# Optimization experiments

Measured on AMD Instinct MI355X. Metric: run time of the kernel, lower is better.

The kernel has to match this reference:

```python
import jax, jax.numpy as jnp
import numpy as np

GAIN_CAP = 0.99
EPS = 1e-4


def _clamp(v):
    # clamp_preserve_grad(v, 0.0, cap) == cap - relu(cap - relu(v))
    r = jax.nn.relu
    return GAIN_CAP - r(GAIN_CAP - r(v))


def _pos(p):
    return jax.nn.softplus(p) + EPS


def setup_inputs() -> dict:
    key = jax.random.key(0)
    ks = jax.random.split(key, 12)
    B, C, H, W, O, M = 4, 128, 256, 256, 16, 32
    return {
        "x": jax.random.normal(ks[0], (B, C, H, W), jnp.float32),
        "steer": jax.random.normal(ks[1], (B, O, H, W), jnp.float32),
        "modulation": jax.random.normal(ks[2], (B, M), jnp.float32),
        "r_center": 0.1 * jax.random.normal(ks[3], (C,), jnp.float32),
        "r_horizontal": 0.1 * jax.random.normal(ks[4], (C,), jnp.float32),
        "r_vertical": 0.1 * jax.random.normal(ks[5], (C,), jnp.float32),
        "r_diag": 0.1 * jax.random.normal(ks[6], (C,), jnp.float32),
        "gain_horizontal": 0.1 * jax.random.normal(ks[7], (C,), jnp.float32),
        "gain_vertical": 0.1 * jax.random.normal(ks[8], (C,), jnp.float32),
        "gain_diag": 0.1 * jax.random.normal(ks[9], (C,), jnp.float32),
        "steer_w": 0.1 * jax.random.normal(ks[10], (4, O), jnp.float32),  # 1x1 conv weight squeezed
        "mod_w": 0.1 * jax.random.normal(ks[11], (3, M), jnp.float32),    # Linear(M,3,bias=False)
    }


def reference(x, steer, modulation, r_center, r_horizontal, r_vertical, r_diag,
              gain_horizontal, gain_vertical, gain_diag, steer_w, mod_w):
    cview = lambda p: p[None, :, None, None]  # (1,C,1,1)
    center = x
    right = jnp.roll(x, -1, axis=-1)
    left = jnp.roll(x, 1, axis=-1)
    up = jnp.roll(x, 1, axis=-2)
    down = jnp.roll(x, -1, axis=-2)
    diag_ne = jnp.roll(x, (-1, -1), axis=(-2, -1))
    diag_sw = jnp.roll(x, (1, 1), axis=(-2, -1))
    diag_nw = jnp.roll(x, (1, -1), axis=(-2, -1))
    diag_se = jnp.roll(x, (-1, 1), axis=(-2, -1))

    r_c = cview(_pos(r_center))
    r_h = cview(_pos(r_horizontal))
    r_v = cview(_pos(r_vertical))
    r_d = cview(_pos(r_diag))

    flow_h = (right - center + (left - center)) / (r_c + r_h)
    flow_v = (up - center + (down - center)) / (r_c + r_v)
    flow_d = (diag_ne - center + (diag_sw - center) + (diag_nw - center) + (diag_se - center)) / (2.0 * (r_c + r_d))

    gh = jnp.tanh(cview(gain_horizontal))
    gv = jnp.tanh(cview(gain_vertical))
    gd = jnp.tanh(cview(gain_diag))

    # modulation gating: [B,3] -> [B,3,1,1]
    delta = jnp.tanh(modulation @ mod_w.T)[:, :, None, None]
    gh = _clamp(gh * (1.0 + 0.1 * delta[:, 0:1]))
    gv = _clamp(gv * (1.0 + 0.1 * delta[:, 1:2]))
    gd = _clamp(gd * (1.0 + 0.1 * delta[:, 2:3]))

    # steer gating: 1x1 conv (no bias) then tanh -> [B,4,H,W]
    steer_fields = jnp.tanh(jnp.einsum('bohw,po->bphw', steer, steer_w))
    gh = _clamp(gh * (1.0 + 0.2 * steer_fields[:, 0:1]))
    gv = _clamp(gv * (1.0 + 0.2 * steer_fields[:, 1:2]))
    gd = _clamp(gd * (1.0 + 0.2 * steer_fields[:, 2:3]))

    update = gh * flow_h + gv * flow_v + gd * flow_d
    return center + update
```

## Files before the change

kernel.cpp:

```cpp
#include <hip/hip_runtime.h>
#include <math.h>

#define GAIN_CAP 0.99f
#define EPSV 1e-4f

static constexpr int B = 4, C = 128, H = 256, W = 256, O = 16, M = 32;
static constexpr int HW = H * W;

typedef float   vfloat4 __attribute__((ext_vector_type(4)));
typedef _Float16 half4v __attribute__((ext_vector_type(4)));
typedef _Float16 half8v __attribute__((ext_vector_type(8)));

static constexpr int SFP_FLOATS = B * HW * 2;
static constexpr int G_SZ = B * C * 3;

__device__ __forceinline__ float softplusf(float x) {
    return log1pf(expf(-fabsf(x))) + fmaxf(x, 0.0f);
}
__device__ __forceinline__ float clampg(float v) {
    return fminf(fmaxf(v, 0.0f), GAIN_CAP);
}
__device__ __forceinline__ float fast_tanh(float x) {
    float e = __expf(2.0f * x);
    return 1.0f - 2.0f * __builtin_amdgcn_rcpf(e + 1.0f);
}

__global__ void __launch_bounds__(256)
steer_kernel(const float* __restrict__ steer,
             const float* __restrict__ steer_w,
             const float* __restrict__ r_center,
             const float* __restrict__ r_h,
             const float* __restrict__ r_v,
             const float* __restrict__ r_d,
             const float* __restrict__ g_h,
             const float* __restrict__ g_v,
             const float* __restrict__ g_d,
             const float* __restrict__ modulation,
             const float* __restrict__ mod_w,
             half4v* __restrict__ sfp,
             float* __restrict__ gains,
             float* __restrict__ invd)
{
    if (blockIdx.x == 0 && threadIdx.x < C) {
        int c = threadIdx.x;
        float rc = softplusf(r_center[c]) + EPSV;
        invd[c * 3 + 0] = 1.0f / (rc + softplusf(r_h[c]) + EPSV);
        invd[c * 3 + 1] = 1.0f / (rc + softplusf(r_v[c]) + EPSV);
        invd[c * 3 + 2] = 1.0f / (2.0f * (rc + softplusf(r_d[c]) + EPSV));
        float th = tanhf(g_h[c]), tv = tanhf(g_v[c]), td = tanhf(g_d[c]);
        for (int b = 0; b < B; ++b) {
            float a0 = 0.f, a1 = 0.f, a2 = 0.f;
#pragma unroll
            for (int m = 0; m < M; ++m) {
                float mv = modulation[b * M + m];
                a0 += mv * mod_w[0 * M + m];
                a1 += mv * mod_w[1 * M + m];
                a2 += mv * mod_w[2 * M + m];
            }
            gains[(b * C + c) * 3 + 0] = clampg(th * (1.0f + 0.1f * tanhf(a0)));
            gains[(b * C + c) * 3 + 1] = clampg(tv * (1.0f + 0.1f * tanhf(a1)));
            gains[(b * C + c) * 3 + 2] = clampg(td * (1.0f + 0.1f * tanhf(a2)));
        }
    }

    int idx = blockIdx.x * 256 + threadIdx.x;
    int b   = idx >> 14;
    int g   = idx & 16383;
    const float4* sp = (const float4*)(steer + ((size_t)b * O << 16)) + g;

    float4 a0 = {0.f, 0.f, 0.f, 0.f}, a1 = a0, a2 = a0;
#pragma unroll
    for (int o = 0; o < O; ++o) {
        float4 v = sp[(size_t)o << 14];
        float w0 = steer_w[o], w1 = steer_w[O + o], w2 = steer_w[2 * O + o];
        a0.x += v.x * w0; a0.y += v.y * w0; a0.z += v.z * w0; a0.w += v.w * w0;
        a1.x += v.x * w1; a1.y += v.y * w1; a1.z += v.z * w1; a1.w += v.w * w1;
        a2.x += v.x * w2; a2.y += v.y * w2; a2.z += v.z * w2; a2.w += v.w * w2;
    }
    half8v oA, oB;
    oA[0] = (_Float16)fast_tanh(a0.x); oA[1] = (_Float16)fast_tanh(a1.x);
    oA[2] = (_Float16)fast_tanh(a2.x); oA[3] = (_Float16)0.f;
    oA[4] = (_Float16)fast_tanh(a0.y); oA[5] = (_Float16)fast_tanh(a1.y);
    oA[6] = (_Float16)fast_tanh(a2.y); oA[7] = (_Float16)0.f;
    oB[0] = (_Float16)fast_tanh(a0.z); oB[1] = (_Float16)fast_tanh(a1.z);
    oB[2] = (_Float16)fast_tanh(a2.z); oB[3] = (_Float16)0.f;
    oB[4] = (_Float16)fast_tanh(a0.w); oB[5] = (_Float16)fast_tanh(a1.w);
    oB[6] = (_Float16)fast_tanh(a2.w); oB[7] = (_Float16)0.f;
    half8v* op = (half8v*)sfp + ((size_t)idx << 1);
    op[0] = oA;
    op[1] = oB;
}

__device__ __forceinline__ vfloat4 row_compute(
    const float4& u, const float4& cc, const float4& d,
    float uL, float uR, float cL, float cR, float dL, float dR,
    float ih, float iv, float idg, float g0, float g1, float g2,
    const float (&s0)[4], const float (&s1)[4], const float (&s2)[4])
{
    float cA[4]  = {cc.x, cc.y, cc.z, cc.w};
    float uA[4]  = {u.x, u.y, u.z, u.w};
    float dA[4]  = {d.x, d.y, d.z, d.w};
    float crA[4] = {cc.y, cc.z, cc.w, cR};
    float clA[4] = {cL, cc.x, cc.y, cc.z};
    float urA[4] = {u.y, u.z, u.w, uR};
    float ulA[4] = {uL, u.x, u.y, u.z};
    float drA[4] = {d.y, d.z, d.w, dR};
    float dlA[4] = {dL, d.x, d.y, d.z};
    vfloat4 o;
#pragma unroll
    for (int j = 0; j < 4; ++j) {
        float fh = (crA[j] + clA[j] - 2.0f * cA[j]) * ih;
        float fv = (uA[j] + dA[j] - 2.0f * cA[j]) * iv;
        float fd = (drA[j] + dlA[j] + urA[j] + ulA[j] - 4.0f * cA[j]) * idg;
        float gh = clampg(g0 * (1.0f + 0.2f * s0[j]));
        float gv = clampg(g1 * (1.0f + 0.2f * s1[j]));
        float gd = clampg(g2 * (1.0f + 0.2f * s2[j]));
        o[j] = cA[j] + gh * fh + gv * fv + gd * fd;
    }
    return o;
}

#define LDROW(p, h) (((const float4*)((p) + ((h) << 8)))[lane])

__global__ void __launch_bounds__(256)
main_kernel(const float* __restrict__ x,
            const half4v* __restrict__ sfp,
            const float* __restrict__ gains,
            const float* __restrict__ invd,
            float* __restrict__ out)
{
    constexpr int RPW = 8;
    int lane  = threadIdx.x & 63;
    int wave  = threadIdx.x >> 6;
    int gid   = blockIdx.x;
    int strip = gid & 7;
    int cg    = (gid >> 3) & 63;
    int b     = gid >> 9;
    int bc0   = b * C + cg * 2;
    int c0    = bc0 & (C - 1);
    int h0    = strip * 32 + wave * RPW;

    const float* p0 = x + ((size_t)bc0 << 16);
    const float* p1 = p0 + HW;
    float* q0 = out + ((size_t)bc0 << 16);
    float* q1 = q0 + HW;
    const half4v* sfb = sfp + ((size_t)b << 16);

    float ih0 = invd[c0 * 3 + 0], iv0 = invd[c0 * 3 + 1], id0 = invd[c0 * 3 + 2];
    float ih1 = invd[c0 * 3 + 3], iv1 = invd[c0 * 3 + 4], id1 = invd[c0 * 3 + 5];
    float g00 = gains[bc0 * 3 + 0], g01 = gains[bc0 * 3 + 1], g02 = gains[bc0 * 3 + 2];
    float g10 = gains[bc0 * 3 + 3], g11 = gains[bc0 * 3 + 4], g12 = gains[bc0 * 3 + 5];

    int lp = (lane + 1) & 63, lm = (lane - 1) & 63;
    int hm = (h0 - 1) & 255;
    int hd = (h0 + 1) & 255;

    float4 u0  = LDROW(p0, hm), u1  = LDROW(p1, hm);
    float4 c0v = LDROW(p0, h0), c1v = LDROW(p1, h0);
    float4 d0  = LDROW(p0, hd), d1  = LDROW(p1, hd);
    const float4* sr0 = (const float4*)(sfb + ((size_t)h0 << 8));
    float4 sA = sr0[2 * lane], sB = sr0[2 * lane + 1];

    float u0R = __shfl(u0.x, lp), u0L = __shfl(u0.w, lm);
    float u1R = __shfl(u1.x, lp), u1L = __shfl(u1.w, lm);
    float c0R = __shfl(c0v.x, lp), c0L = __shfl(c0v.w, lm);
    float c1R = __shfl(c1v.x, lp), c1L = __shfl(c1v.w, lm);

#pragma unroll
    for (int r = 0; r < RPW; ++r) {
        int h = h0 + r;

        float4 nd0 = d0, nd1 = d1, nsA = sA, nsB = sB;
        if (r + 1 < RPW) {
            int h2 = (h + 2) & 255;
            nd0 = LDROW(p0, h2);
            nd1 = LDROW(p1, h2);
            const float4* srn = (const float4*)(sfb + ((size_t)(h + 1) << 8));
            nsA = srn[2 * lane];
            nsB = srn[2 * lane + 1];
        }

        float d0R = __shfl(d0.x, lp), d0L = __shfl(d0.w, lm);
        float d1R = __shfl(d1.x, lp), d1L = __shfl(d1.w, lm);

        half8v hA = __builtin_bit_cast(half8v, sA);
        half8v hB = __builtin_bit_cast(half8v, sB);
        float s0[4], s1[4], s2[4];
        s0[0] = (float)hA[0]; s1[0] = (float)hA[1]; s2[0] = (float)hA[2];
        s0[1] = (float)hA[4]; s1[1] = (float)hA[5]; s2[1] = (float)hA[6];
        s0[2] = (float)hB[0]; s1[2] = (float)hB[1]; s2[2] = (float)hB[2];
        s0[3] = (float)hB[4]; s1[3] = (float)hB[5]; s2[3] = (float)hB[6];

        vfloat4 o0 = row_compute(u0, c0v, d0, u0L, u0R, c0L, c0R, d0L, d0R,
                                 ih0, iv0, id0, g00, g01, g02, s0, s1, s2);
        vfloat4 o1 = row_compute(u1, c1v, d1, u1L, u1R, c1L, c1R, d1L, d1R,
                                 ih1, iv1, id1, g10, g11, g12, s0, s1, s2);
        __builtin_nontemporal_store(o0, (vfloat4*)(q0 + (h << 8)) + lane);
        __builtin_nontemporal_store(o1, (vfloat4*)(q1 + (h << 8)) + lane);

        u0 = c0v; u0R = c0R; u0L = c0L;
        u1 = c1v; u1R = c1R; u1L = c1L;
        c0v = d0; c0R = d0R; c0L = d0L;
        c1v = d1; c1R = d1R; c1L = d1L;
        d0 = nd0; d1 = nd1;
        sA = nsA; sB = nsB;
    }
}

extern "C" void kernel_launch(void* const* d_in, const int* in_sizes, int n_in,
                              void* d_out, int out_size, void* d_ws, size_t ws_size,
                              hipStream_t stream) {
    const float* x          = (const float*)d_in[0];
    const float* steer      = (const float*)d_in[1];
    const float* modulation = (const float*)d_in[2];
    const float* r_center   = (const float*)d_in[3];
    const float* r_horiz    = (const float*)d_in[4];
    const float* r_vert     = (const float*)d_in[5];
    const float* r_diag     = (const float*)d_in[6];
    const float* g_horiz    = (const float*)d_in[7];
    const float* g_vert     = (const float*)d_in[8];
    const float* g_diag     = (const float*)d_in[9];
    const float* steer_w    = (const float*)d_in[10];
    const float* mod_w      = (const float*)d_in[11];

    float* ws     = (float*)d_ws;
    half4v* sfp   = (half4v*)ws;
    float* gains  = ws + SFP_FLOATS;
    float* invd   = gains + G_SZ;
    float* out    = (float*)d_out;

    steer_kernel<<<(B * HW / 4) / 256, 256, 0, stream>>>(
        steer, steer_w, r_center, r_horiz, r_vert, r_diag,
        g_horiz, g_vert, g_diag, modulation, mod_w, sfp, gains, invd);
    main_kernel<<<B * (C / 2) * 8, 256, 0, stream>>>(x, sfp, gains, invd, out);
}
```

Measured before the change: 275.3 us.

## Share steer-field rows across waves via LDS with channel-split block mapping

```diff
diff --git a/kernel.cpp b/kernel.cpp
--- a/kernel.cpp
+++ b/kernel.cpp
@@ -122,7 +122,7 @@
 
 #define LDROW(p, h) (((const float4*)((p) + ((h) << 8)))[lane])
 
-__global__ void __launch_bounds__(256)
+__global__ void __launch_bounds__(256, 6)
 main_kernel(const float* __restrict__ x,
             const half4v* __restrict__ sfp,
             const float* __restrict__ gains,
@@ -130,21 +130,33 @@
             float* __restrict__ out)
 {
     constexpr int RPW = 8;
+    __shared__ float4 smA[RPW][64];
+    __shared__ float4 smB[RPW][64];
+
     int lane  = threadIdx.x & 63;
     int wave  = threadIdx.x >> 6;
     int gid   = blockIdx.x;
-    int strip = gid & 7;
-    int cg    = (gid >> 3) & 63;
+    int strip = gid & 31;
+    int cgrp  = (gid >> 5) & 15;
     int b     = gid >> 9;
-    int bc0   = b * C + cg * 2;
+    int h0    = strip * 8;
+    int bc0   = b * C + cgrp * 8 + wave * 2;
     int c0    = bc0 & (C - 1);
-    int h0    = strip * 32 + wave * RPW;
+
+    {
+        const float4* s4 = (const float4*)(sfp + ((size_t)b << 16) + ((size_t)h0 << 8));
+        for (int i = threadIdx.x; i < RPW * 128; i += 256) {
+            int r = i >> 7, k = i & 127;
+            float4 v = s4[i];
+            if (k & 1) smB[r][k >> 1] = v;
+            else       smA[r][k >> 1] = v;
+        }
+    }
 
     const float* p0 = x + ((size_t)bc0 << 16);
     const float* p1 = p0 + HW;
     float* q0 = out + ((size_t)bc0 << 16);
     float* q1 = q0 + HW;
-    const half4v* sfb = sfp + ((size_t)b << 16);
 
     float ih0 = invd[c0 * 3 + 0], iv0 = invd[c0 * 3 + 1], id0 = invd[c0 * 3 + 2];
     float ih1 = invd[c0 * 3 + 3], iv1 = invd[c0 * 3 + 4], id1 = invd[c0 * 3 + 5];
@@ -158,27 +170,27 @@
     float4 u0  = LDROW(p0, hm), u1  = LDROW(p1, hm);
     float4 c0v = LDROW(p0, h0), c1v = LDROW(p1, h0);
     float4 d0  = LDROW(p0, hd), d1  = LDROW(p1, hd);
-    const float4* sr0 = (const float4*)(sfb + ((size_t)h0 << 8));
-    float4 sA = sr0[2 * lane], sB = sr0[2 * lane + 1];
 
     float u0R = __shfl(u0.x, lp), u0L = __shfl(u0.w, lm);
     float u1R = __shfl(u1.x, lp), u1L = __shfl(u1.w, lm);
     float c0R = __shfl(c0v.x, lp), c0L = __shfl(c0v.w, lm);
     float c1R = __shfl(c1v.x, lp), c1L = __shfl(c1v.w, lm);
 
+    __syncthreads();
+
 #pragma unroll
     for (int r = 0; r < RPW; ++r) {
         int h = h0 + r;
 
-        float4 nd0 = d0, nd1 = d1, nsA = sA, nsB = sB;
+        float4 nd0 = d0, nd1 = d1;
         if (r + 1 < RPW) {
             int h2 = (h + 2) & 255;
             nd0 = LDROW(p0, h2);
             nd1 = LDROW(p1, h2);
-            const float4* srn = (const float4*)(sfb + ((size_t)(h + 1) << 8));
-            nsA = srn[2 * lane];
-            nsB = srn[2 * lane + 1];
         }
+
+        float4 sA = smA[r][lane];
+        float4 sB = smB[r][lane];
 
         float d0R = __shfl(d0.x, lp), d0L = __shfl(d0.w, lm);
         float d1R = __shfl(d1.x, lp), d1L = __shfl(d1.w, lm);
@@ -203,7 +215,6 @@
         c0v = d0; c0R = d0R; c0L = d0L;
         c1v = d1; c1R = d1R; c1L = d1L;
         d0 = nd0; d1 = nd1;
-        sA = nsA; sB = nsB;
     }
 }
 
@@ -232,5 +243,5 @@
     steer_kernel<<<(B * HW / 4) / 256, 256, 0, stream>>>(
         steer, steer_w, r_center, r_horiz, r_vert, r_diag,
         g_horiz, g_vert, g_diag, modulation, mod_w, sfp, gains, invd);
-    main_kernel<<<B * (C / 2) * 8, 256, 0, stream>>>(x, sfp, gains, invd, out);
-}
+    main_kernel<<<B * (C / 8) * 32, 256, 0, stream>>>(x, sfp, gains, invd, out);
+}
```

Result: slower. 366.7 us (+33.2%).
